# Kernel optimization log

Hardware: AMD Instinct MI355X
Metric: run time of the kernel (lower is better)

The kernel has to match this reference:

```python
import jax, jax.numpy as jnp
import numpy as np

PATCH = 7
STRIDE = 1


def extract_patches(im, p=PATCH, stride=STRIDE):
    # im: [b, c, h, w] -> patches [b, N, c*p*p] (torch.nn.Unfold-style layout)
    pt = jax.lax.conv_general_dilated_patches(
        im, filter_shape=(p, p), window_strides=(stride, stride), padding='VALID')
    # pt: [b, c*p*p, h', w']
    b, d = pt.shape[0], pt.shape[1]
    return pt.reshape(b, d, -1).transpose(0, 2, 1)  # [b, N, d]


def coherence_swd(xp, yp, rand):
    # xp, yp: [N, d]; rand: [d, P]
    r = rand / jnp.std(rand, axis=0, keepdims=True, ddof=1)  # torch.std is unbiased
    px = xp @ r  # [N, P]
    py = yp @ r  # [N, P]
    ix = jnp.argsort(px, axis=0).T  # [P, N]
    iy = jnp.argsort(py, axis=0).T  # [P, N]
    # Gather full patch vectors by per-projection sorted order, L1 distance.
    # xp[ix]: [P, N, d] -- the big irregular-gather intermediate.
    diff = jnp.abs(xp[ix] - yp[iy])  # [P, N, d]
    # loss = (1/P) * sum_p mean(|...|_p); each term has identical size -> plain mean
    return diff.mean()


def setup_inputs() -> dict:
    key = jax.random.key(0)
    k1, k2, k3 = jax.random.split(key, 3)
    b, c, h, w = 1, 3, 96, 96
    d = c * PATCH * PATCH  # 147
    num_proj = 256
    x = jax.random.normal(k1, (b, c, h, w), dtype=jnp.float32)
    y = jax.random.normal(k2, (b, c, h, w), dtype=jnp.float32)
    rand = jax.random.normal(k3, (d, num_proj), dtype=jnp.float32)
    return {"x": x, "y": y, "rand": rand}


def reference(x, y, rand):
    x_patches = extract_patches(x)  # [b, N, d]
    y_patches = extract_patches(y)
    losses = jax.vmap(coherence_swd, in_axes=(0, 0, None))(x_patches, y_patches, rand)  # [b]
    return losses.mean()  # batch_reduction='mean'
```

## Files before the change

kernel.cpp:

```cpp
#include <hip/hip_runtime.h>

#define HH 96
#define WW 96
#define OH 90
#define OW 90
#define NPATCH 8100
#define DD 147
#define NPROJ 256
#define TN 64
#define KPAD 160
#define NKS 5
#define SORT_T 1024
#define NBUCK 4096
#define KPT 8
#define PGRP 16
#define NCH 64
#define KPB2 128
#define QSCALE 21.25f

typedef short bf16x8 __attribute__((ext_vector_type(8)));
typedef float f32x4 __attribute__((ext_vector_type(4)));

__device__ __forceinline__ unsigned short bf16_rne(float f) {
    unsigned u = __builtin_bit_cast(unsigned, f);
    u += 0x7FFFu + ((u >> 16) & 1u);
    return (unsigned short)(u >> 16);
}
__device__ __forceinline__ float bf16_f(unsigned short h) {
    return __builtin_bit_cast(float, (unsigned)h << 16);
}

__device__ __forceinline__ unsigned sad4(unsigned x, unsigned y, unsigned a) {
    unsigned d;
    asm("v_sad_u8 %0, %1, %2, %3" : "=v"(d) : "v"(x), "v"(y), "v"(a));
    return d;
}

__global__ __launch_bounds__(512, 2)
void patch_proj_kernel(const float* __restrict__ x, const float* __restrict__ y,
                       const float* __restrict__ rnd,
                       int* __restrict__ xm8, int* __restrict__ ym8,
                       int* __restrict__ xt8, int* __restrict__ yt8,
                       float* __restrict__ pxT, float* __restrict__ pyT,
                       float* __restrict__ out)
{
    __shared__ unsigned short sh[2][TN * KPAD];
    const int tid = threadIdx.x;
    const int n0 = blockIdx.x * TN;
    const int img = blockIdx.y;
    const float* __restrict__ src = img ? y : x;
    int* __restrict__ m8 = img ? ym8 : xm8;
    int* __restrict__ t8 = img ? yt8 : xt8;
    float* __restrict__ pT = img ? pyT : pxT;
    if (blockIdx.x == 0 && img == 0 && tid == 0) out[0] = 0.0f;

    const int wv = tid >> 6, lane = tid & 63;
    const int cl = lane & 15, qk = lane >> 4;

    bf16x8 bh[NKS][2], bl[NKS][2];
#pragma unroll
    for (int ks = 0; ks < NKS; ++ks) {
#pragma unroll
        for (int nt = 0; nt < 2; ++nt) {
            const int col = wv * 32 + nt * 16 + cl;
#pragma unroll
            for (int j = 0; j < 8; ++j) {
                const int k = ks * 32 + qk * 8 + j;
                const float v = (k < DD) ? rnd[k * NPROJ + col] : 0.f;
                const unsigned short h = bf16_rne(v);
                bh[ks][nt][j] = (short)h;
                bl[ks][nt][j] = (short)bf16_rne(v - bf16_f(h));
            }
        }
    }

    for (int idx = tid; idx < TN * 40; idx += 512) {
        const int t = idx / 40;
        const int u = idx - t * 40;
        const int n = n0 + t;
        const int d0 = 4 * u;
        unsigned short h4[4], l4[4];
#pragma unroll
        for (int e = 0; e < 4; ++e) {
            const int d = d0 + e;
            float v = 0.f;
            if (n < NPATCH && d < DD) {
                const int oy = n / OW, ox = n - oy * OW;
                const int c  = d / 49, r  = d - c * 49;
                const int di = r / 7,  dj = r - di * 7;
                v = src[c * (HH * WW) + (oy + di) * WW + (ox + dj)];
            }
            const unsigned short hi = bf16_rne(v);
            h4[e] = hi;
            l4[e] = bf16_rne(v - bf16_f(hi));
        }
        const int mt = t >> 4, r16 = t & 15;
        const int ks = d0 >> 5, q = (d0 & 31) >> 3, jb = d0 & 7;
        const int fidx = (((mt * NKS + ks) * 4 + q) * 16 + r16) * 8 + jb;
        ushort4 hv; hv.x = h4[0]; hv.y = h4[1]; hv.z = h4[2]; hv.w = h4[3];
        ushort4 lv; lv.x = l4[0]; lv.y = l4[1]; lv.z = l4[2]; lv.w = l4[3];
        *(ushort4*)&sh[0][fidx] = hv;
        *(ushort4*)&sh[1][fidx] = lv;
        if (n < NPATCH) {
            unsigned w = 0;
#pragma unroll
            for (int e = 0; e < 4; ++e) {
                float f = fmaf(bf16_f(h4[e]), QSCALE, 128.5f);
                f = fminf(fmaxf(f, 0.f), 255.f);
                w |= ((unsigned)f) << (8 * e);
            }
            if (u < 32) m8[(size_t)n * 32 + u] = (int)w;
            else        t8[(size_t)n * 8 + (u - 32)] = (int)w;
        }
    }
    __syncthreads();

    f32x4 acc[4][2];
#pragma unroll
    for (int mt = 0; mt < 4; ++mt)
#pragma unroll
        for (int nt = 0; nt < 2; ++nt)
            acc[mt][nt] = (f32x4){0.f, 0.f, 0.f, 0.f};

#pragma unroll
    for (int ks = 0; ks < NKS; ++ks) {
#pragma unroll
        for (int mt = 0; mt < 4; ++mt) {
            const int base = ((mt * NKS + ks) * 64 + lane) * 8;
            const bf16x8 ah = *(const bf16x8*)&sh[0][base];
            const bf16x8 al = *(const bf16x8*)&sh[1][base];
#pragma unroll
            for (int nt = 0; nt < 2; ++nt) {
                acc[mt][nt] = __builtin_amdgcn_mfma_f32_16x16x32_bf16(ah, bh[ks][nt], acc[mt][nt], 0, 0, 0);
                acc[mt][nt] = __builtin_amdgcn_mfma_f32_16x16x32_bf16(ah, bl[ks][nt], acc[mt][nt], 0, 0, 0);
                acc[mt][nt] = __builtin_amdgcn_mfma_f32_16x16x32_bf16(al, bh[ks][nt], acc[mt][nt], 0, 0, 0);
            }
        }
    }

#pragma unroll
    for (int mt = 0; mt < 4; ++mt) {
        const int patch = n0 + mt * 16 + qk * 4;
#pragma unroll
        for (int nt = 0; nt < 2; ++nt) {
            const int proj = wv * 32 + nt * 16 + cl;
            float* rowp = pT + (size_t)proj * NPATCH + patch;
            if (patch + 3 < NPATCH) {
                *(f32x4*)rowp = acc[mt][nt];
            } else {
#pragma unroll
                for (int e = 0; e < 4; ++e)
                    if (patch + e < NPATCH) rowp[e] = acc[mt][nt][e];
            }
        }
    }
}

__global__ __launch_bounds__(SORT_T, 4)
void rank_kernel(const float* __restrict__ pT,
                 unsigned short* __restrict__ partner)
{
    __shared__ unsigned hist[NBUCK];
    __shared__ unsigned cnt[NBUCK];
    __shared__ float    skey[8192];
    __shared__ unsigned short iyl[8192];
    __shared__ unsigned wsum[16];
    const int p = blockIdx.x;
    const int tid = threadIdx.x;
    const int lane = tid & 63;
    const int wid = tid >> 6;

    unsigned short xr[KPT];

#pragma unroll
    for (int pass = 0; pass < 2; ++pass) {
        const float* col = pT + (size_t)(p + pass * NPROJ) * NPATCH;

        ((uint4*)hist)[tid] = make_uint4(0, 0, 0, 0);
        ((uint4*)cnt)[tid]  = make_uint4(0, 0, 0, 0);
        if (pass == 1) {
            ((uint4*)iyl)[tid] = make_uint4(0xFFFFFFFFu, 0xFFFFFFFFu,
                                            0xFFFFFFFFu, 0xFFFFFFFFu);
            if (tid < 1024) ((uint4*)iyl)[tid + 1024] = make_uint4(
                0xFFFFFFFFu, 0xFFFFFFFFu, 0xFFFFFFFFu, 0xFFFFFFFFu);
        }
        __syncthreads();

        float k[KPT];
        int bk[KPT];
#pragma unroll
        for (int t = 0; t < KPT; ++t) {
            const int i = tid + SORT_T * t;
            if (i < NPATCH) {
                const float v = col[i];
                k[t] = v;
                int b = (int)((v + 51.2f) * 40.0f);
                b = b < 0 ? 0 : (b > NBUCK - 1 ? NBUCK - 1 : b);
                bk[t] = b;
                atomicAdd(&hist[b], 1u);
            } else {
                k[t] = 0.f;
                bk[t] = -1;
            }
        }
        __syncthreads();

        {
            const int b0 = tid * 4;
            unsigned h[4];
#pragma unroll
            for (int q = 0; q < 4; ++q) h[q] = hist[b0 + q];
            unsigned tsum = h[0] + h[1] + h[2] + h[3];
            unsigned acc = tsum;
#pragma unroll
            for (int d = 1; d < 64; d <<= 1) {
                const unsigned v = __shfl_up(acc, d, 64);
                if (lane >= d) acc += v;
            }
            const unsigned wexcl = acc - tsum;
            if (lane == 63) wsum[wid] = acc;
            __syncthreads();
            if (tid == 0) {
                unsigned roff = 0;
#pragma unroll
                for (int w = 0; w < 16; ++w) {
                    const unsigned tt = wsum[w];
                    wsum[w] = roff;
                    roff += tt;
                }
            }
            __syncthreads();
            unsigned run = wsum[wid] + wexcl;
#pragma unroll
            for (int q = 0; q < 4; ++q) { cnt[b0 + q] = run; run += h[q]; }
        }
        __syncthreads();

#pragma unroll
        for (int t = 0; t < KPT; ++t) {
            if (bk[t] >= 0) {
                const unsigned pos = atomicAdd(&cnt[bk[t]], 1u);
                skey[pos] = k[t];
            }
        }
        __syncthreads();

#pragma unroll
        for (int t = 0; t < KPT; ++t) {
            if (bk[t] < 0) continue;
            const int b = bk[t];
            const unsigned end = cnt[b];
            const unsigned cb = hist[b];
            const unsigned start = end - cb;
            const float myk = k[t];
            unsigned r = start;
            for (unsigned s2 = start; s2 < end; ++s2)
                r += (skey[s2] < myk) ? 1u : 0u;
            if (pass == 0) {
                xr[t] = (unsigned short)r;
            } else {
                iyl[r] = (unsigned short)(tid + SORT_T * t);
            }
        }
        __syncthreads();
    }

#pragma unroll
    for (int t = 0; t < KPT; ++t) {
        const int i = tid + SORT_T * t;
        if (i >= NPATCH) continue;
        const unsigned short j = iyl[xr[t]];
        partner[(size_t)p * NPATCH + i] =
            (j < NPATCH) ? j : (unsigned short)(NPATCH - 1);
    }
}

__global__ __launch_bounds__(256, 4)
void reduce_kernel(const uint4* __restrict__ xm8, const uint4* __restrict__ ym8,
                   const uint4* __restrict__ xt8, const uint4* __restrict__ yt8,
                   const unsigned short* __restrict__ partner,
                   float* __restrict__ out)
{
    __shared__ unsigned short sp[PGRP * KPB2];
    const int p0 = blockIdx.y * PGRP;
    const int i0 = blockIdx.x * KPB2;
    const int iend = min(i0 + KPB2, NPATCH);
    const int tid = threadIdx.x;
    const int wave = tid >> 6, lane = tid & 63;

    for (int idx = tid; idx < PGRP * KPB2; idx += 256) {
        const int pp = idx >> 7, r = idx & 127;
        int src = i0 + r;
        src = src < NPATCH ? src : NPATCH - 1;
        sp[idx] = partner[(size_t)(p0 + pp) * NPATCH + src];
    }
    __syncthreads();

    unsigned uacc = 0;

    {
        const int g = lane >> 3;
        const int u = lane & 7;
#pragma unroll
        for (int it = 0; it < 4; ++it) {
            const int i = i0 + wave * 8 + it * 32;
            const uint4 xa = xm8[(size_t)i * 8 + lane];
            int jj[PGRP];
#pragma unroll
            for (int pp = 0; pp < PGRP; ++pp)
                jj[pp] = sp[pp * KPB2 + (i - i0) + g];
            uint4 ya[PGRP];
#pragma unroll
            for (int pp = 0; pp < PGRP; ++pp)
                ya[pp] = ym8[(size_t)jj[pp] * 8 + u];
            unsigned s0 = 0, s1 = 0;
#pragma unroll
            for (int pp = 0; pp < PGRP; ++pp) {
                s0 = sad4(xa.x, ya[pp].x, s0);
                s1 = sad4(xa.y, ya[pp].y, s1);
                s0 = sad4(xa.z, ya[pp].z, s0);
                s1 = sad4(xa.w, ya[pp].w, s1);
            }
            uacc += (i + g < iend) ? (s0 + s1) : 0u;
        }
    }

    {
        const int g2 = lane >> 1;
        const int u2 = lane & 1;
        const int i2 = i0 + wave * 32;
        const uint4 xa = xt8[(size_t)i2 * 2 + lane];
        int jj[PGRP];
#pragma unroll
        for (int pp = 0; pp < PGRP; ++pp)
            jj[pp] = sp[pp * KPB2 + (i2 - i0) + g2];
        uint4 ya[PGRP];
#pragma unroll
        for (int pp = 0; pp < PGRP; ++pp)
            ya[pp] = yt8[(size_t)jj[pp] * 2 + u2];
        unsigned s0 = 0, s1 = 0;
#pragma unroll
        for (int pp = 0; pp < PGRP; ++pp) {
            s0 = sad4(xa.x, ya[pp].x, s0);
            s1 = sad4(xa.y, ya[pp].y, s1);
            s0 = sad4(xa.z, ya[pp].z, s0);
            s1 = sad4(xa.w, ya[pp].w, s1);
        }
        uacc += (i2 + g2 < iend) ? (s0 + s1) : 0u;
    }

    float facc = (float)uacc;
#pragma unroll
    for (int o = 32; o > 0; o >>= 1) facc += __shfl_down(facc, o, 64);

    __shared__ float sred[4];
    if (lane == 0) sred[wave] = facc;
    __syncthreads();
    if (tid == 0) {
        const float s = sred[0] + sred[1] + sred[2] + sred[3];
        const float scale = (float)(1.0 / ((double)NPROJ * (double)NPATCH *
                                           (double)DD * (double)QSCALE));
        atomicAdd(out, s * scale);
    }
}

extern "C" void kernel_launch(void* const* d_in, const int* in_sizes, int n_in,
                              void* d_out, int out_size, void* d_ws, size_t ws_size,
                              hipStream_t stream)
{
    const float* x   = (const float*)d_in[0];
    const float* y   = (const float*)d_in[1];
    const float* rnd = (const float*)d_in[2];

    char* ws = (char*)d_ws;
    int* xm8 = (int*)(ws + 0);
    int* ym8 = (int*)(ws + 1036800);
    int* xt8 = (int*)(ws + 2073600);
    int* yt8 = (int*)(ws + 2332800);
    float* pxT = (float*)(ws + 2592000);
    float* pyT = (float*)(ws + 10886400);
    unsigned short* partner = (unsigned short*)(ws + 19180800);
    float* out = (float*)d_out;

    hipLaunchKernelGGL(patch_proj_kernel, dim3((NPATCH + TN - 1) / TN, 2), dim3(512), 0, stream,
                       x, y, rnd, xm8, ym8, xt8, yt8, pxT, pyT, out);
    hipLaunchKernelGGL(rank_kernel, dim3(NPROJ), dim3(SORT_T), 0, stream,
                       pxT, partner);
    hipLaunchKernelGGL(reduce_kernel, dim3(NCH, NPROJ / PGRP), dim3(256), 0, stream,
                       (const uint4*)xm8, (const uint4*)ym8,
                       (const uint4*)xt8, (const uint4*)yt8, partner, out);
}
```

Baseline: 120.1 us.

## Rank x and y projections concurrently in split halves; precompute patch offsets

The rank kernel now splits its 1024 threads into two halves that bucket-sort the x and y projection columns at the same time, each with its own histogram, count and key arrays, instead of doing two sequential passes. This removes one pass's worth of barriers and serial latency, but doubles shared-memory use (around 80KB), which can lower occupancy, and gives each thread 16 keys instead of 8. The patch-extraction stage also precomputes the per-dimension image offsets into a shared table, which removes the per-element integer divisions.

```diff
diff --git a/kernel.cpp b/kernel.cpp
--- a/kernel.cpp
+++ b/kernel.cpp
@@ -10,9 +10,7 @@
 #define TN 64
 #define KPAD 160
 #define NKS 5
-#define SORT_T 1024
 #define NBUCK 4096
-#define KPT 8
 #define PGRP 16
 #define NCH 64
 #define KPB2 128
@@ -45,6 +43,7 @@
                        float* __restrict__ out)
 {
     __shared__ unsigned short sh[2][TN * KPAD];
+    __shared__ int offt[KPAD];
     const int tid = threadIdx.x;
     const int n0 = blockIdx.x * TN;
     const int img = blockIdx.y;
@@ -57,6 +56,16 @@
     const int wv = tid >> 6, lane = tid & 63;
     const int cl = lane & 15, qk = lane >> 4;
 
+    if (tid < KPAD) {
+        int o = -1;
+        if (tid < DD) {
+            const int c = tid / 49, r = tid - c * 49;
+            const int di = r / 7, dj = r - di * 7;
+            o = c * (HH * WW) + di * WW + dj;
+        }
+        offt[tid] = o;
+    }
+
     bf16x8 bh[NKS][2], bl[NKS][2];
 #pragma unroll
     for (int ks = 0; ks < NKS; ++ks) {
@@ -73,44 +82,49 @@
             }
         }
     }
-
-    for (int idx = tid; idx < TN * 40; idx += 512) {
-        const int t = idx / 40;
-        const int u = idx - t * 40;
+    __syncthreads();
+
+    {
+        const int t = tid >> 3;
+        const int u0 = tid & 7;
         const int n = n0 + t;
-        const int d0 = 4 * u;
-        unsigned short h4[4], l4[4];
-#pragma unroll
-        for (int e = 0; e < 4; ++e) {
-            const int d = d0 + e;
-            float v = 0.f;
-            if (n < NPATCH && d < DD) {
-                const int oy = n / OW, ox = n - oy * OW;
-                const int c  = d / 49, r  = d - c * 49;
-                const int di = r / 7,  dj = r - di * 7;
-                v = src[c * (HH * WW) + (oy + di) * WW + (ox + dj)];
-            }
-            const unsigned short hi = bf16_rne(v);
-            h4[e] = hi;
-            l4[e] = bf16_rne(v - bf16_f(hi));
+        const bool nok = n < NPATCH;
+        int baseoff = 0;
+        if (nok) {
+            const int oy = n / OW, ox = n - oy * OW;
+            baseoff = oy * WW + ox;
         }
         const int mt = t >> 4, r16 = t & 15;
-        const int ks = d0 >> 5, q = (d0 & 31) >> 3, jb = d0 & 7;
-        const int fidx = (((mt * NKS + ks) * 4 + q) * 16 + r16) * 8 + jb;
-        ushort4 hv; hv.x = h4[0]; hv.y = h4[1]; hv.z = h4[2]; hv.w = h4[3];
-        ushort4 lv; lv.x = l4[0]; lv.y = l4[1]; lv.z = l4[2]; lv.w = l4[3];
-        *(ushort4*)&sh[0][fidx] = hv;
-        *(ushort4*)&sh[1][fidx] = lv;
-        if (n < NPATCH) {
-            unsigned w = 0;
+#pragma unroll
+        for (int it = 0; it < 5; ++it) {
+            const int u = u0 + 8 * it;
+            const int d0 = 4 * u;
+            unsigned short h4[4], l4[4];
 #pragma unroll
             for (int e = 0; e < 4; ++e) {
-                float f = fmaf(bf16_f(h4[e]), QSCALE, 128.5f);
-                f = fminf(fmaxf(f, 0.f), 255.f);
-                w |= ((unsigned)f) << (8 * e);
-            }
-            if (u < 32) m8[(size_t)n * 32 + u] = (int)w;
-            else        t8[(size_t)n * 8 + (u - 32)] = (int)w;
+                const int o = offt[d0 + e];
+                const float v = (nok && o >= 0) ? src[baseoff + o] : 0.f;
+                const unsigned short hi = bf16_rne(v);
+                h4[e] = hi;
+                l4[e] = bf16_rne(v - bf16_f(hi));
+            }
+            const int ks = d0 >> 5, q = (d0 & 31) >> 3, jb = d0 & 7;
+            const int fidx = (((mt * NKS + ks) * 4 + q) * 16 + r16) * 8 + jb;
+            ushort4 hv; hv.x = h4[0]; hv.y = h4[1]; hv.z = h4[2]; hv.w = h4[3];
+            ushort4 lv; lv.x = l4[0]; lv.y = l4[1]; lv.z = l4[2]; lv.w = l4[3];
+            *(ushort4*)&sh[0][fidx] = hv;
+            *(ushort4*)&sh[1][fidx] = lv;
+            if (nok) {
+                unsigned w = 0;
+#pragma unroll
+                for (int e = 0; e < 4; ++e) {
+                    float f = fmaf(bf16_f(h4[e]), QSCALE, 128.5f);
+                    f = fminf(fmaxf(f, 0.f), 255.f);
+                    w |= ((unsigned)f) << (8 * e);
+                }
+                if (u < 32) m8[(size_t)n * 32 + u] = (int)w;
+                else        t8[(size_t)n * 8 + (u - 32)] = (int)w;
+            }
         }
     }
     __syncthreads();
@@ -156,122 +170,128 @@
     }
 }
 
-__global__ __launch_bounds__(SORT_T, 4)
+__global__ __launch_bounds__(1024, 4)
 void rank_kernel(const float* __restrict__ pT,
                  unsigned short* __restrict__ partner)
 {
-    __shared__ unsigned hist[NBUCK];
-    __shared__ unsigned cnt[NBUCK];
-    __shared__ float    skey[8192];
+    __shared__ unsigned hist[2][NBUCK];
+    __shared__ unsigned cnt[2][NBUCK];
+    __shared__ float    skey[2][8192];
     __shared__ unsigned short iyl[8192];
-    __shared__ unsigned wsum[16];
+    __shared__ unsigned wsum[2][8];
     const int p = blockIdx.x;
     const int tid = threadIdx.x;
+    const int half = tid >> 9;
+    const int t5 = tid & 511;
     const int lane = tid & 63;
-    const int wid = tid >> 6;
-
-    unsigned short xr[KPT];
-
-#pragma unroll
-    for (int pass = 0; pass < 2; ++pass) {
-        const float* col = pT + (size_t)(p + pass * NPROJ) * NPATCH;
-
-        ((uint4*)hist)[tid] = make_uint4(0, 0, 0, 0);
-        ((uint4*)cnt)[tid]  = make_uint4(0, 0, 0, 0);
-        if (pass == 1) {
-            ((uint4*)iyl)[tid] = make_uint4(0xFFFFFFFFu, 0xFFFFFFFFu,
-                                            0xFFFFFFFFu, 0xFFFFFFFFu);
-            if (tid < 1024) ((uint4*)iyl)[tid + 1024] = make_uint4(
-                0xFFFFFFFFu, 0xFFFFFFFFu, 0xFFFFFFFFu, 0xFFFFFFFFu);
-        }
+    const int wid5 = t5 >> 6;
+
+    const float* __restrict__ col = pT + (size_t)(p + half * NPROJ) * NPATCH;
+    unsigned* H  = hist[half];
+    unsigned* Cn = cnt[half];
+    float*    SK = skey[half];
+
+    {
+        const uint4 z = make_uint4(0, 0, 0, 0);
+        ((uint4*)H)[t5]        = z;
+        ((uint4*)H)[t5 + 512]  = z;
+        ((uint4*)Cn)[t5]       = z;
+        ((uint4*)Cn)[t5 + 512] = z;
+        if (half) {
+            const uint4 f = make_uint4(~0u, ~0u, ~0u, ~0u);
+            ((uint4*)iyl)[t5]       = f;
+            ((uint4*)iyl)[t5 + 512] = f;
+        }
+    }
+    __syncthreads();
+
+    float k[16];
+    int bk[16];
+#pragma unroll
+    for (int t = 0; t < 16; ++t) {
+        const int i = t5 + 512 * t;
+        if (i < NPATCH) {
+            const float v = col[i];
+            k[t] = v;
+            int b = (int)((v + 51.2f) * 40.0f);
+            b = b < 0 ? 0 : (b > NBUCK - 1 ? NBUCK - 1 : b);
+            bk[t] = b;
+            atomicAdd(&H[b], 1u);
+        } else {
+            k[t] = 0.f;
+            bk[t] = -1;
+        }
+    }
+    __syncthreads();
+
+    {
+        const int b0 = t5 * 8;
+        unsigned h[8];
+#pragma unroll
+        for (int q = 0; q < 8; ++q) h[q] = H[b0 + q];
+        unsigned tsum = 0;
+#pragma unroll
+        for (int q = 0; q < 8; ++q) tsum += h[q];
+        unsigned acc = tsum;
+#pragma unroll
+        for (int d = 1; d < 64; d <<= 1) {
+            const unsigned v = __shfl_up(acc, d, 64);
+            if (lane >= d) acc += v;
+        }
+        const unsigned wexcl = acc - tsum;
+        if (lane == 63) wsum[half][wid5] = acc;
         __syncthreads();
-
-        float k[KPT];
-        int bk[KPT];
-#pragma unroll
-        for (int t = 0; t < KPT; ++t) {
-            const int i = tid + SORT_T * t;
-            if (i < NPATCH) {
-                const float v = col[i];
-                k[t] = v;
-                int b = (int)((v + 51.2f) * 40.0f);
-                b = b < 0 ? 0 : (b > NBUCK - 1 ? NBUCK - 1 : b);
-                bk[t] = b;
-                atomicAdd(&hist[b], 1u);
-            } else {
-                k[t] = 0.f;
-                bk[t] = -1;
+        if (t5 == 0) {
+            unsigned roff = 0;
+#pragma unroll
+            for (int w = 0; w < 8; ++w) {
+                const unsigned tt = wsum[half][w];
+                wsum[half][w] = roff;
+                roff += tt;
             }
         }
         __syncthreads();
-
-        {
-            const int b0 = tid * 4;
-            unsigned h[4];
-#pragma unroll
-            for (int q = 0; q < 4; ++q) h[q] = hist[b0 + q];
-            unsigned tsum = h[0] + h[1] + h[2] + h[3];
-            unsigned acc = tsum;
-#pragma unroll
-            for (int d = 1; d < 64; d <<= 1) {
-                const unsigned v = __shfl_up(acc, d, 64);
-                if (lane >= d) acc += v;
-            }
-            const unsigned wexcl = acc - tsum;
-            if (lane == 63) wsum[wid] = acc;
-            __syncthreads();
-            if (tid == 0) {
-                unsigned roff = 0;
-#pragma unroll
-                for (int w = 0; w < 16; ++w) {
-                    const unsigned tt = wsum[w];
-                    wsum[w] = roff;
-                    roff += tt;
-                }
-            }
-            __syncthreads();
-            unsigned run = wsum[wid] + wexcl;
-#pragma unroll
-            for (int q = 0; q < 4; ++q) { cnt[b0 + q] = run; run += h[q]; }
-        }
-        __syncthreads();
-
-#pragma unroll
-        for (int t = 0; t < KPT; ++t) {
-            if (bk[t] >= 0) {
-                const unsigned pos = atomicAdd(&cnt[bk[t]], 1u);
-                skey[pos] = k[t];
-            }
-        }
-        __syncthreads();
-
-#pragma unroll
-        for (int t = 0; t < KPT; ++t) {
-            if (bk[t] < 0) continue;
-            const int b = bk[t];
-            const unsigned end = cnt[b];
-            const unsigned cb = hist[b];
-            const unsigned start = end - cb;
-            const float myk = k[t];
-            unsigned r = start;
-            for (unsigned s2 = start; s2 < end; ++s2)
-                r += (skey[s2] < myk) ? 1u : 0u;
-            if (pass == 0) {
-                xr[t] = (unsigned short)r;
-            } else {
-                iyl[r] = (unsigned short)(tid + SORT_T * t);
-            }
-        }
-        __syncthreads();
-    }
-
-#pragma unroll
-    for (int t = 0; t < KPT; ++t) {
-        const int i = tid + SORT_T * t;
-        if (i >= NPATCH) continue;
-        const unsigned short j = iyl[xr[t]];
-        partner[(size_t)p * NPATCH + i] =
-            (j < NPATCH) ? j : (unsigned short)(NPATCH - 1);
+        unsigned run = wsum[half][wid5] + wexcl;
+#pragma unroll
+        for (int q = 0; q < 8; ++q) { Cn[b0 + q] = run; run += h[q]; }
+    }
+    __syncthreads();
+
+#pragma unroll
+    for (int t = 0; t < 16; ++t) {
+        if (bk[t] >= 0) {
+            const unsigned pos = atomicAdd(&Cn[bk[t]], 1u);
+            SK[pos] = k[t];
+        }
+    }
+    __syncthreads();
+
+    unsigned short xr[16];
+#pragma unroll
+    for (int t = 0; t < 16; ++t) {
+        if (bk[t] < 0) continue;
+        const int b = bk[t];
+        const unsigned end = Cn[b];
+        const unsigned cb = H[b];
+        const unsigned start = end - cb;
+        const float myk = k[t];
+        unsigned r = start;
+        for (unsigned s2 = start; s2 < end; ++s2)
+            r += (SK[s2] < myk) ? 1u : 0u;
+        if (half == 0) xr[t] = (unsigned short)r;
+        else           iyl[r] = (unsigned short)(t5 + 512 * t);
+    }
+    __syncthreads();
+
+    if (half == 0) {
+#pragma unroll
+        for (int t = 0; t < 16; ++t) {
+            const int i = t5 + 512 * t;
+            if (i >= NPATCH) continue;
+            const unsigned short j = iyl[xr[t]];
+            partner[(size_t)p * NPATCH + i] =
+                (j < NPATCH) ? j : (unsigned short)(NPATCH - 1);
+        }
     }
 }
 
@@ -384,7 +404,7 @@
 
     hipLaunchKernelGGL(patch_proj_kernel, dim3((NPATCH + TN - 1) / TN, 2), dim3(512), 0, stream,
                        x, y, rnd, xm8, ym8, xt8, yt8, pxT, pyT, out);
-    hipLaunchKernelGGL(rank_kernel, dim3(NPROJ), dim3(SORT_T), 0, stream,
+    hipLaunchKernelGGL(rank_kernel, dim3(NPROJ), dim3(1024), 0, stream,
                        pxT, partner);
     hipLaunchKernelGGL(reduce_kernel, dim3(NCH, NPROJ / PGRP), dim3(256), 0, stream,
                        (const uint4*)xm8, (const uint4*)ym8,
```

After: 120.9 us. No clear change (+0.7%).
